# Performance work log

Hardware: AMD Instinct MI355X
Metric: run time of the kernel (lower is better)

The kernel has to match this reference:

```python
import jax, jax.numpy as jnp
import numpy as np

ALPHA = 0.2  # LeakyReLU negative slope
MASK_VAL = -1e12


def setup_inputs() -> dict:
    key = jax.random.key(0)
    k1, k2, k3, k4 = jax.random.split(key, 4)
    B, N, F_in, F_out = 16, 1024, 128, 64
    inp = jax.random.normal(k1, (B, N, F_in), dtype=jnp.float32)
    adj = jax.random.randint(k2, (B, N, N), 0, 2, dtype=jnp.int32)
    W = jax.random.normal(k3, (F_in, F_out), dtype=jnp.float32) * (1.414 / np.sqrt(F_in))
    a = jax.random.normal(k4, (2 * F_out, 1), dtype=jnp.float32) * (1.414 / np.sqrt(2 * F_out))
    return {"inp": inp, "adj": adj, "W": W, "a": a}


def reference(inp, adj, W, a):
    # inp: [B, N, F_in], adj: [B, N, N], W: [F_in, F_out], a: [2*F_out, 1]
    F_out = W.shape[1]
    h = jnp.einsum('bnf,fo->bno', inp, W)  # [B, N, F_out]
    # e_ij = LeakyReLU(a1 . h_i + a2 . h_j)  (equivalent to concat-then-matmul)
    a1 = a[:F_out, 0]  # [F_out]
    a2 = a[F_out:, 0]  # [F_out]
    e = jax.nn.leaky_relu(
        (h @ a1)[:, :, None] + (h @ a2)[:, None, :], negative_slope=ALPHA
    )  # [B, N, N]
    scores = jnp.where(adj > 0, e, MASK_VAL)
    attention = jax.nn.softmax(scores, axis=-1)  # [B, N, N]
    # dropout with p=0.0 / eval mode -> identity
    h_prime = jnp.einsum('bij,bjo->bio', attention, h)  # [B, N, F_out]
    return jax.nn.elu(h_prime)  # concat=True
```

## Files before the change

### kernel.cpp

```cpp
#include <hip/hip_runtime.h>
#include <cstdint>

#define BB   16
#define NN   1024
#define FIN  128
#define FOUT 64
#define ALPHA_S 0.2f
#define LOG2E 1.44269504f

typedef float    f32x4 __attribute__((ext_vector_type(4)));
typedef _Float16 half8 __attribute__((ext_vector_type(8)));
typedef _Float16 half4 __attribute__((ext_vector_type(4)));
typedef __fp16   pk2   __attribute__((ext_vector_type(2)));
typedef __fp16   pk4   __attribute__((ext_vector_type(4)));
typedef __fp16   pk8   __attribute__((ext_vector_type(8)));

__device__ __forceinline__ float fast_exp2(float x){
  float r; asm("v_exp_f32 %0, %1" : "=v"(r) : "v"(x)); return r;
}

__global__ __launch_bounds__(256) void k_proj(const float* __restrict__ inp,
                                              const float* __restrict__ W,
                                              const float* __restrict__ a,
                                              _Float16* __restrict__ hT,
                                              float* __restrict__ s1,
                                              float* __restrict__ s2){
  __shared__ float red1[4][16];
  __shared__ float red2[4][16];
  const int t = threadIdx.x;
  const int w = t >> 6, lane = t & 63;
  const int m16 = lane & 15, g = lane >> 4;
  const int i0 = blockIdx.x * 16;
  const int b  = i0 >> 10;
  const int j0 = i0 & 1023;
  const int c0 = w * 16;

  const float* arow = inp + (size_t)(i0 + m16) * FIN;

  f32x4 acc = {0.f, 0.f, 0.f, 0.f};
  #pragma unroll
  for (int kk = 0; kk < 4; ++kk){
    const int kbase = kk * 32 + g * 8;
    float4 av0 = *(const float4*)(arow + kbase);
    float4 av1 = *(const float4*)(arow + kbase + 4);
    const float av[8] = {av0.x, av0.y, av0.z, av0.w, av1.x, av1.y, av1.z, av1.w};
    half8 ah, al;
    #pragma unroll
    for (int j = 0; j < 8; ++j){
      _Float16 h = (_Float16)av[j];
      ah[j] = h;
      al[j] = (_Float16)(av[j] - (float)h);
    }
    half8 bh, bl;
    #pragma unroll
    for (int j = 0; j < 8; ++j){
      float wv = W[(kbase + j) * FOUT + c0 + m16];
      _Float16 h = (_Float16)wv;
      bh[j] = h;
      bl[j] = (_Float16)(wv - (float)h);
    }
    acc = __builtin_amdgcn_mfma_f32_16x16x32_f16(ah, bh, acc, 0, 0, 0);
    acc = __builtin_amdgcn_mfma_f32_16x16x32_f16(ah, bl, acc, 0, 0, 0);
    acc = __builtin_amdgcn_mfma_f32_16x16x32_f16(al, bh, acc, 0, 0, 0);
  }

  const float a1c = a[c0 + m16];
  const float a2c = a[FOUT + c0 + m16];
  f32x4 p1, p2;
  #pragma unroll
  for (int q = 0; q < 4; ++q){ p1[q] = acc[q] * a1c; p2[q] = acc[q] * a2c; }
  #pragma unroll
  for (int off = 1; off < 16; off <<= 1){
    #pragma unroll
    for (int q = 0; q < 4; ++q){
      p1[q] += __shfl_xor(p1[q], off, 64);
      p2[q] += __shfl_xor(p2[q], off, 64);
    }
  }
  if (m16 == 0){
    #pragma unroll
    for (int q = 0; q < 4; ++q){
      red1[w][g * 4 + q] = p1[q];
      red2[w][g * 4 + q] = p2[q];
    }
  }

  half4 hv;
  #pragma unroll
  for (int q = 0; q < 4; ++q) hv[q] = (_Float16)acc[q];
  size_t idx = (size_t)b * 65536 + (size_t)(j0 >> 5) * 2048
             + (size_t)(c0 + m16) * 32 + (size_t)(j0 & 31) + (size_t)g * 4;
  *(half4*)(hT + idx) = hv;

  __syncthreads();
  if (t < 16){
    s1[i0 + t] = (red1[0][t] + red1[1][t] + red1[2][t] + red1[3][t]) * LOG2E;
    s2[i0 + t] = (red2[0][t] + red2[1][t] + red2[2][t] + red2[3][t]) * LOG2E;
  }
}

__global__ __launch_bounds__(256, 4) void k_attn(const int* __restrict__ adj,
                                                 const _Float16* __restrict__ hT,
                                                 const float* __restrict__ s1,
                                                 const float* __restrict__ s2,
                                                 float* __restrict__ out){
  __shared__ float s2_s[NN];
  __shared__ float redmax[4][16];
  __shared__ float redl[4][16];
  __shared__ float csum[4][1088];

  const int t = threadIdx.x;
  const int w = t >> 6, lane = t & 63;
  const int m16 = lane & 15, g = lane >> 4;
  const int b  = blockIdx.x >> 6;
  const int i0 = (blockIdx.x & 63) * 16;
  const int jb = w * 256;

  *(float4*)&s2_s[jb + lane * 4] = *(const float4*)(s2 + b * NN + jb + lane * 4);

  const int* arow = adj + ((size_t)(b * NN + i0 + m16)) * NN + jb + g * 8;
  int4 A0[8], A1[8];
  #pragma unroll
  for (int kk = 0; kk < 8; ++kk){
    A0[kk] = *(const int4*)(arow + kk * 32);
    A1[kk] = *(const int4*)(arow + kk * 32 + 4);
  }

  const float s1i = s1[b * NN + i0 + m16];

  unsigned mask_lo = 0u, mask_hi = 0u;
  float mxp = -3.0e38f;
  #pragma unroll
  for (int kk = 0; kk < 8; ++kk){
    float4 sA = *(const float4*)&s2_s[jb + kk * 32 + g * 8];
    float4 sB = *(const float4*)&s2_s[jb + kk * 32 + g * 8 + 4];
    unsigned bits = 0u;
    bits |= (A0[kk].x > 0) ? 1u   : 0u;  mxp = fmaxf(mxp, A0[kk].x > 0 ? sA.x : -3.0e38f);
    bits |= (A0[kk].y > 0) ? 2u   : 0u;  mxp = fmaxf(mxp, A0[kk].y > 0 ? sA.y : -3.0e38f);
    bits |= (A0[kk].z > 0) ? 4u   : 0u;  mxp = fmaxf(mxp, A0[kk].z > 0 ? sA.z : -3.0e38f);
    bits |= (A0[kk].w > 0) ? 8u   : 0u;  mxp = fmaxf(mxp, A0[kk].w > 0 ? sA.w : -3.0e38f);
    bits |= (A1[kk].x > 0) ? 16u  : 0u;  mxp = fmaxf(mxp, A1[kk].x > 0 ? sB.x : -3.0e38f);
    bits |= (A1[kk].y > 0) ? 32u  : 0u;  mxp = fmaxf(mxp, A1[kk].y > 0 ? sB.y : -3.0e38f);
    bits |= (A1[kk].z > 0) ? 64u  : 0u;  mxp = fmaxf(mxp, A1[kk].z > 0 ? sB.z : -3.0e38f);
    bits |= (A1[kk].w > 0) ? 128u : 0u;  mxp = fmaxf(mxp, A1[kk].w > 0 ? sB.w : -3.0e38f);
    if (kk < 4) mask_lo |= bits << (kk * 8);
    else        mask_hi |= bits << ((kk - 4) * 8);
  }

  mxp = fmaxf(mxp, __shfl_xor(mxp, 16, 64));
  mxp = fmaxf(mxp, __shfl_xor(mxp, 32, 64));
  mxp = fmaxf(mxp, -1.0e30f);
  const float xm   = s1i + mxp;
  const float mrow = fmaxf(xm, ALPHA_S * xm);
  if (g == 0) redmax[w][m16] = mrow;
  const float s1m = s1i - mrow;
  const float c2  = ALPHA_S * s1i - mrow;

  f32x4 acc0 = {0,0,0,0}, acc1 = {0,0,0,0}, acc2 = {0,0,0,0}, acc3 = {0,0,0,0};
  float psum = 0.f;
  const _Float16* bhp = hT + (size_t)b * 65536 + (size_t)(w * 8) * 2048
                      + (size_t)m16 * 32 + (size_t)g * 8;

  #pragma unroll
  for (int kk = 0; kk < 8; ++kk){
    float4 sA = *(const float4*)&s2_s[jb + kk * 32 + g * 8];
    float4 sB = *(const float4*)&s2_s[jb + kk * 32 + g * 8 + 4];
    const unsigned bits = (kk < 4) ? (mask_lo >> (kk * 8)) : (mask_hi >> ((kk - 4) * 8));
    const float sv[8] = {sA.x, sA.y, sA.z, sA.w, sB.x, sB.y, sB.z, sB.w};
    float p[8];
    #pragma unroll
    for (int u = 0; u < 8; ++u){
      float e = fast_exp2(fmaxf(s1m + sv[u], fmaf(ALPHA_S, sv[u], c2)));
      p[u] = ((bits >> u) & 1u) ? e : 0.0f;
    }
    psum += ((p[0] + p[1]) + (p[2] + p[3])) + ((p[4] + p[5]) + (p[6] + p[7]));

    pk2 q0 = __builtin_amdgcn_cvt_pkrtz(p[0], p[1]);
    pk2 q1 = __builtin_amdgcn_cvt_pkrtz(p[2], p[3]);
    pk2 q2 = __builtin_amdgcn_cvt_pkrtz(p[4], p[5]);
    pk2 q3 = __builtin_amdgcn_cvt_pkrtz(p[6], p[7]);
    pk4 l0 = __builtin_shufflevector(q0, q1, 0, 1, 2, 3);
    pk4 l1 = __builtin_shufflevector(q2, q3, 0, 1, 2, 3);
    half8 af = __builtin_bit_cast(half8,
                 __builtin_shufflevector(l0, l1, 0, 1, 2, 3, 4, 5, 6, 7));

    half8 b0 = *(const half8*)(bhp + kk * 2048);
    half8 b1 = *(const half8*)(bhp + kk * 2048 + 512);
    half8 b2 = *(const half8*)(bhp + kk * 2048 + 1024);
    half8 b3 = *(const half8*)(bhp + kk * 2048 + 1536);
    acc0 = __builtin_amdgcn_mfma_f32_16x16x32_f16(af, b0, acc0, 0, 0, 0);
    acc1 = __builtin_amdgcn_mfma_f32_16x16x32_f16(af, b1, acc1, 0, 0, 0);
    acc2 = __builtin_amdgcn_mfma_f32_16x16x32_f16(af, b2, acc2, 0, 0, 0);
    acc3 = __builtin_amdgcn_mfma_f32_16x16x32_f16(af, b3, acc3, 0, 0, 0);
  }

  psum += __shfl_xor(psum, 16, 64);
  psum += __shfl_xor(psum, 32, 64);
  if (g == 0) redl[w][m16] = psum;

  #pragma unroll
  for (int q = 0; q < 4; ++q){
    csum[w][(g * 4 + q) * 68 +  0 + m16] = acc0[q];
    csum[w][(g * 4 + q) * 68 + 16 + m16] = acc1[q];
    csum[w][(g * 4 + q) * 68 + 32 + m16] = acc2[q];
    csum[w][(g * 4 + q) * 68 + 48 + m16] = acc3[q];
  }
  __syncthreads();

  const int r  = t >> 4;
  const int c4 = (t & 15) * 4;
  const float m0 = redmax[0][r], m1 = redmax[1][r];
  const float m2 = redmax[2][r], m3 = redmax[3][r];
  const float mg = fmaxf(fmaxf(m0, m1), fmaxf(m2, m3));
  const float f0 = fast_exp2(m0 - mg), f1 = fast_exp2(m1 - mg);
  const float f2 = fast_exp2(m2 - mg), f3 = fast_exp2(m3 - mg);

  f32x4 c0v = *(const f32x4*)&csum[0][r * 68 + c4];
  f32x4 c1v = *(const f32x4*)&csum[1][r * 68 + c4];
  f32x4 c2v = *(const f32x4*)&csum[2][r * 68 + c4];
  f32x4 c3v = *(const f32x4*)&csum[3][r * 68 + c4];
  f32x4 sum;
  #pragma unroll
  for (int u = 0; u < 4; ++u)
    sum[u] = c0v[u] * f0 + c1v[u] * f1 + c2v[u] * f2 + c3v[u] * f3;

  const float l = redl[0][r] * f0 + redl[1][r] * f1
                + redl[2][r] * f2 + redl[3][r] * f3;
  const float linv = (l > 0.f) ? __builtin_amdgcn_rcpf(l) : 0.f;
  f32x4 o;
  #pragma unroll
  for (int u = 0; u < 4; ++u){
    float v = sum[u] * linv;
    o[u] = v > 0.f ? v : __expf(v) - 1.0f;
  }
  *(f32x4*)(out + ((size_t)(b * NN + i0 + r)) * FOUT + c4) = o;
}

extern "C" void kernel_launch(void* const* d_in, const int* in_sizes, int n_in,
                              void* d_out, int out_size, void* d_ws, size_t ws_size,
                              hipStream_t stream) {
  (void)in_sizes; (void)n_in; (void)out_size; (void)ws_size;
  const float* inp = (const float*)d_in[0];
  const int*   adj = (const int*)d_in[1];
  const float* W   = (const float*)d_in[2];
  const float* a   = (const float*)d_in[3];
  float* outp = (float*)d_out;

  _Float16* hT = (_Float16*)d_ws;
  float* s1 = (float*)(hT + (size_t)BB * 65536);
  float* s2 = s1 + BB * NN;

  k_proj<<<BB * NN / 16, 256, 0, stream>>>(inp, W, a, hT, s1, s2);
  k_attn<<<BB * (NN / 16), 256, 0, stream>>>(adj, hT, s1, s2, outp);
}
```

Measured before the change: 115.1 us.

## Process four row tiles per projection block with W reuse and prefetch

The projection kernel now handles 64 rows per block instead of 16. It loads and splits W into fp16 hi/lo fragments once per block and reuses them across four 16-row tiles. The input rows for the next tile are prefetched into registers while the current tile computes. The reduction buffers are double-buffered so that one barrier per tile is enough, at the cost of higher register use and a grid four times smaller.

```diff
diff --git a/kernel.cpp b/kernel.cpp
--- a/kernel.cpp
+++ b/kernel.cpp
@@ -25,77 +25,105 @@
                                               _Float16* __restrict__ hT,
                                               float* __restrict__ s1,
                                               float* __restrict__ s2){
-  __shared__ float red1[4][16];
-  __shared__ float red2[4][16];
+  __shared__ float red1[2][4][16];
+  __shared__ float red2[2][4][16];
   const int t = threadIdx.x;
   const int w = t >> 6, lane = t & 63;
   const int m16 = lane & 15, g = lane >> 4;
-  const int i0 = blockIdx.x * 16;
-  const int b  = i0 >> 10;
-  const int j0 = i0 & 1023;
-  const int c0 = w * 16;
-
-  const float* arow = inp + (size_t)(i0 + m16) * FIN;
-
-  f32x4 acc = {0.f, 0.f, 0.f, 0.f};
+  const int bi0 = blockIdx.x * 64;
+  const int b   = bi0 >> 10;
+  const int c0  = w * 16;
+
+  half8 bhf[4], blf[4];
   #pragma unroll
   for (int kk = 0; kk < 4; ++kk){
     const int kbase = kk * 32 + g * 8;
-    float4 av0 = *(const float4*)(arow + kbase);
-    float4 av1 = *(const float4*)(arow + kbase + 4);
-    const float av[8] = {av0.x, av0.y, av0.z, av0.w, av1.x, av1.y, av1.z, av1.w};
-    half8 ah, al;
-    #pragma unroll
-    for (int j = 0; j < 8; ++j){
-      _Float16 h = (_Float16)av[j];
-      ah[j] = h;
-      al[j] = (_Float16)(av[j] - (float)h);
-    }
-    half8 bh, bl;
     #pragma unroll
     for (int j = 0; j < 8; ++j){
       float wv = W[(kbase + j) * FOUT + c0 + m16];
       _Float16 h = (_Float16)wv;
-      bh[j] = h;
-      bl[j] = (_Float16)(wv - (float)h);
-    }
-    acc = __builtin_amdgcn_mfma_f32_16x16x32_f16(ah, bh, acc, 0, 0, 0);
-    acc = __builtin_amdgcn_mfma_f32_16x16x32_f16(ah, bl, acc, 0, 0, 0);
-    acc = __builtin_amdgcn_mfma_f32_16x16x32_f16(al, bh, acc, 0, 0, 0);
+      bhf[kk][j] = h;
+      blf[kk][j] = (_Float16)(wv - (float)h);
+    }
   }
 
   const float a1c = a[c0 + m16];
   const float a2c = a[FOUT + c0 + m16];
-  f32x4 p1, p2;
-  #pragma unroll
-  for (int q = 0; q < 4; ++q){ p1[q] = acc[q] * a1c; p2[q] = acc[q] * a2c; }
-  #pragma unroll
-  for (int off = 1; off < 16; off <<= 1){
-    #pragma unroll
-    for (int q = 0; q < 4; ++q){
-      p1[q] += __shfl_xor(p1[q], off, 64);
-      p2[q] += __shfl_xor(p2[q], off, 64);
-    }
-  }
-  if (m16 == 0){
-    #pragma unroll
-    for (int q = 0; q < 4; ++q){
-      red1[w][g * 4 + q] = p1[q];
-      red2[w][g * 4 + q] = p2[q];
-    }
-  }
-
-  half4 hv;
-  #pragma unroll
-  for (int q = 0; q < 4; ++q) hv[q] = (_Float16)acc[q];
-  size_t idx = (size_t)b * 65536 + (size_t)(j0 >> 5) * 2048
-             + (size_t)(c0 + m16) * 32 + (size_t)(j0 & 31) + (size_t)g * 4;
-  *(half4*)(hT + idx) = hv;
-
-  __syncthreads();
-  if (t < 16){
-    s1[i0 + t] = (red1[0][t] + red1[1][t] + red1[2][t] + red1[3][t]) * LOG2E;
-    s2[i0 + t] = (red2[0][t] + red2[1][t] + red2[2][t] + red2[3][t]) * LOG2E;
+
+  float4 pv0[2][4], pv1[2][4];
+  {
+    const float* ar = inp + (size_t)(bi0 + m16) * FIN;
+    #pragma unroll
+    for (int kk = 0; kk < 4; ++kk){
+      pv0[0][kk] = *(const float4*)(ar + kk * 32 + g * 8);
+      pv1[0][kk] = *(const float4*)(ar + kk * 32 + g * 8 + 4);
+    }
+  }
+
+  #pragma unroll
+  for (int rt = 0; rt < 4; ++rt){
+    const int ph = rt & 1;
+    const int i0 = bi0 + rt * 16;
+    const int j0 = i0 & 1023;
+
+    if (rt < 3){
+      const float* ar = inp + (size_t)(i0 + 16 + m16) * FIN;
+      #pragma unroll
+      for (int kk = 0; kk < 4; ++kk){
+        pv0[ph ^ 1][kk] = *(const float4*)(ar + kk * 32 + g * 8);
+        pv1[ph ^ 1][kk] = *(const float4*)(ar + kk * 32 + g * 8 + 4);
+      }
+    }
+
+    f32x4 acc = {0.f, 0.f, 0.f, 0.f};
+    #pragma unroll
+    for (int kk = 0; kk < 4; ++kk){
+      const float4 a0 = pv0[ph][kk], a1 = pv1[ph][kk];
+      const float av[8] = {a0.x, a0.y, a0.z, a0.w, a1.x, a1.y, a1.z, a1.w};
+      half8 ah, al;
+      #pragma unroll
+      for (int j = 0; j < 8; ++j){
+        _Float16 h = (_Float16)av[j];
+        ah[j] = h;
+        al[j] = (_Float16)(av[j] - (float)h);
+      }
+      acc = __builtin_amdgcn_mfma_f32_16x16x32_f16(ah, bhf[kk], acc, 0, 0, 0);
+      acc = __builtin_amdgcn_mfma_f32_16x16x32_f16(ah, blf[kk], acc, 0, 0, 0);
+      acc = __builtin_amdgcn_mfma_f32_16x16x32_f16(al, bhf[kk], acc, 0, 0, 0);
+    }
+
+    half4 hv;
+    #pragma unroll
+    for (int q = 0; q < 4; ++q) hv[q] = (_Float16)acc[q];
+    size_t idx = (size_t)b * 65536 + (size_t)(j0 >> 5) * 2048
+               + (size_t)(c0 + m16) * 32 + (size_t)(j0 & 31) + (size_t)g * 4;
+    *(half4*)(hT + idx) = hv;
+
+    f32x4 p1, p2;
+    #pragma unroll
+    for (int q = 0; q < 4; ++q){ p1[q] = acc[q] * a1c; p2[q] = acc[q] * a2c; }
+    #pragma unroll
+    for (int off = 1; off < 16; off <<= 1){
+      #pragma unroll
+      for (int q = 0; q < 4; ++q){
+        p1[q] += __shfl_xor(p1[q], off, 64);
+        p2[q] += __shfl_xor(p2[q], off, 64);
+      }
+    }
+    if (m16 == 0){
+      #pragma unroll
+      for (int q = 0; q < 4; ++q){
+        red1[ph][w][g * 4 + q] = p1[q];
+        red2[ph][w][g * 4 + q] = p2[q];
+      }
+    }
+    __syncthreads();
+    if (t < 16){
+      s1[i0 + t] = (red1[ph][0][t] + red1[ph][1][t]
+                  + red1[ph][2][t] + red1[ph][3][t]) * LOG2E;
+      s2[i0 + t] = (red2[ph][0][t] + red2[ph][1][t]
+                  + red2[ph][2][t] + red2[ph][3][t]) * LOG2E;
+    }
   }
 }
 
@@ -250,6 +278,6 @@
   float* s1 = (float*)(hT + (size_t)BB * 65536);
   float* s2 = s1 + BB * NN;
 
-  k_proj<<<BB * NN / 16, 256, 0, stream>>>(inp, W, a, hT, s1, s2);
+  k_proj<<<BB * NN / 64, 256, 0, stream>>>(inp, W, a, hT, s1, s2);
   k_attn<<<BB * (NN / 16), 256, 0, stream>>>(adj, hT, s1, s2, outp);
 }
```

Result: no change. 115.9 us (+0.7%).

## Move adjacency bitmask packing from attention kernel into projection kernel

Applied to the files above, without the earlier changes.

The projection kernel now also reads the int32 adjacency matrix, packs each row into bitmasks, and writes them to workspace. The attention kernel reads the compact uint2 masks instead of the full adjacency. The intent is to move the large adjacency read into the projection kernel, where it can overlap with the projection loads and math, and to lighten the attention kernel. The total adjacency traffic stays the same, and a small extra mask write and read is added.

```diff
diff --git a/kernel.cpp b/kernel.cpp
--- a/kernel.cpp
+++ b/kernel.cpp
@@ -22,9 +22,11 @@
 __global__ __launch_bounds__(256) void k_proj(const float* __restrict__ inp,
                                               const float* __restrict__ W,
                                               const float* __restrict__ a,
+                                              const int* __restrict__ adj,
                                               _Float16* __restrict__ hT,
                                               float* __restrict__ s1,
-                                              float* __restrict__ s2){
+                                              float* __restrict__ s2,
+                                              uint2* __restrict__ msk){
   __shared__ float red1[4][16];
   __shared__ float red2[4][16];
   const int t = threadIdx.x;
@@ -35,29 +37,42 @@
   const int j0 = i0 & 1023;
   const int c0 = w * 16;
 
-  const float* arow = inp + (size_t)(i0 + m16) * FIN;
+  const float* arow_i = inp + (size_t)(i0 + m16) * FIN;
+  float4 iv0[4], iv1[4];
+  #pragma unroll
+  for (int kk = 0; kk < 4; ++kk){
+    iv0[kk] = *(const float4*)(arow_i + kk * 32 + g * 8);
+    iv1[kk] = *(const float4*)(arow_i + kk * 32 + g * 8 + 4);
+  }
+  float wv[4][8];
+  #pragma unroll
+  for (int kk = 0; kk < 4; ++kk){
+    #pragma unroll
+    for (int j = 0; j < 8; ++j)
+      wv[kk][j] = W[(kk * 32 + g * 8 + j) * FOUT + c0 + m16];
+  }
+  const int* arow_a = adj + (size_t)(i0 + m16) * NN + w * 256 + g * 8;
+  int4 A0[8], A1[8];
+  #pragma unroll
+  for (int kk = 0; kk < 8; ++kk){
+    A0[kk] = *(const int4*)(arow_a + kk * 32);
+    A1[kk] = *(const int4*)(arow_a + kk * 32 + 4);
+  }
 
   f32x4 acc = {0.f, 0.f, 0.f, 0.f};
   #pragma unroll
   for (int kk = 0; kk < 4; ++kk){
-    const int kbase = kk * 32 + g * 8;
-    float4 av0 = *(const float4*)(arow + kbase);
-    float4 av1 = *(const float4*)(arow + kbase + 4);
-    const float av[8] = {av0.x, av0.y, av0.z, av0.w, av1.x, av1.y, av1.z, av1.w};
-    half8 ah, al;
+    const float av[8] = {iv0[kk].x, iv0[kk].y, iv0[kk].z, iv0[kk].w,
+                         iv1[kk].x, iv1[kk].y, iv1[kk].z, iv1[kk].w};
+    half8 ah, al, bh, bl;
     #pragma unroll
     for (int j = 0; j < 8; ++j){
       _Float16 h = (_Float16)av[j];
       ah[j] = h;
       al[j] = (_Float16)(av[j] - (float)h);
-    }
-    half8 bh, bl;
-    #pragma unroll
-    for (int j = 0; j < 8; ++j){
-      float wv = W[(kbase + j) * FOUT + c0 + m16];
-      _Float16 h = (_Float16)wv;
-      bh[j] = h;
-      bl[j] = (_Float16)(wv - (float)h);
+      _Float16 hw = (_Float16)wv[kk][j];
+      bh[j] = hw;
+      bl[j] = (_Float16)(wv[kk][j] - (float)hw);
     }
     acc = __builtin_amdgcn_mfma_f32_16x16x32_f16(ah, bh, acc, 0, 0, 0);
     acc = __builtin_amdgcn_mfma_f32_16x16x32_f16(ah, bl, acc, 0, 0, 0);
@@ -97,9 +112,26 @@
     s1[i0 + t] = (red1[0][t] + red1[1][t] + red1[2][t] + red1[3][t]) * LOG2E;
     s2[i0 + t] = (red2[0][t] + red2[1][t] + red2[2][t] + red2[3][t]) * LOG2E;
   }
-}
-
-__global__ __launch_bounds__(256, 4) void k_attn(const int* __restrict__ adj,
+
+  unsigned mask_lo = 0u, mask_hi = 0u;
+  #pragma unroll
+  for (int kk = 0; kk < 8; ++kk){
+    unsigned bits = 0u;
+    bits |= (A0[kk].x > 0) ? 1u   : 0u;
+    bits |= (A0[kk].y > 0) ? 2u   : 0u;
+    bits |= (A0[kk].z > 0) ? 4u   : 0u;
+    bits |= (A0[kk].w > 0) ? 8u   : 0u;
+    bits |= (A1[kk].x > 0) ? 16u  : 0u;
+    bits |= (A1[kk].y > 0) ? 32u  : 0u;
+    bits |= (A1[kk].z > 0) ? 64u  : 0u;
+    bits |= (A1[kk].w > 0) ? 128u : 0u;
+    if (kk < 4) mask_lo |= bits << (kk * 8);
+    else        mask_hi |= bits << ((kk - 4) * 8);
+  }
+  msk[(size_t)blockIdx.x * 256 + t] = make_uint2(mask_lo, mask_hi);
+}
+
+__global__ __launch_bounds__(256, 4) void k_attn(const uint2* __restrict__ msk,
                                                  const _Float16* __restrict__ hT,
                                                  const float* __restrict__ s1,
                                                  const float* __restrict__ s2,
@@ -118,33 +150,23 @@
 
   *(float4*)&s2_s[jb + lane * 4] = *(const float4*)(s2 + b * NN + jb + lane * 4);
 
-  const int* arow = adj + ((size_t)(b * NN + i0 + m16)) * NN + jb + g * 8;
-  int4 A0[8], A1[8];
-  #pragma unroll
-  for (int kk = 0; kk < 8; ++kk){
-    A0[kk] = *(const int4*)(arow + kk * 32);
-    A1[kk] = *(const int4*)(arow + kk * 32 + 4);
-  }
-
+  const uint2 mk  = msk[(size_t)blockIdx.x * 256 + t];
   const float s1i = s1[b * NN + i0 + m16];
 
-  unsigned mask_lo = 0u, mask_hi = 0u;
   float mxp = -3.0e38f;
   #pragma unroll
   for (int kk = 0; kk < 8; ++kk){
     float4 sA = *(const float4*)&s2_s[jb + kk * 32 + g * 8];
     float4 sB = *(const float4*)&s2_s[jb + kk * 32 + g * 8 + 4];
-    unsigned bits = 0u;
-    bits |= (A0[kk].x > 0) ? 1u   : 0u;  mxp = fmaxf(mxp, A0[kk].x > 0 ? sA.x : -3.0e38f);
-    bits |= (A0[kk].y > 0) ? 2u   : 0u;  mxp = fmaxf(mxp, A0[kk].y > 0 ? sA.y : -3.0e38f);
-    bits |= (A0[kk].z > 0) ? 4u   : 0u;  mxp = fmaxf(mxp, A0[kk].z > 0 ? sA.z : -3.0e38f);
-    bits |= (A0[kk].w > 0) ? 8u   : 0u;  mxp = fmaxf(mxp, A0[kk].w > 0 ? sA.w : -3.0e38f);
-    bits |= (A1[kk].x > 0) ? 16u  : 0u;  mxp = fmaxf(mxp, A1[kk].x > 0 ? sB.x : -3.0e38f);
-    bits |= (A1[kk].y > 0) ? 32u  : 0u;  mxp = fmaxf(mxp, A1[kk].y > 0 ? sB.y : -3.0e38f);
-    bits |= (A1[kk].z > 0) ? 64u  : 0u;  mxp = fmaxf(mxp, A1[kk].z > 0 ? sB.z : -3.0e38f);
-    bits |= (A1[kk].w > 0) ? 128u : 0u;  mxp = fmaxf(mxp, A1[kk].w > 0 ? sB.w : -3.0e38f);
-    if (kk < 4) mask_lo |= bits << (kk * 8);
-    else        mask_hi |= bits << ((kk - 4) * 8);
+    const unsigned bits = (kk < 4) ? (mk.x >> (kk * 8)) : (mk.y >> ((kk - 4) * 8));
+    mxp = fmaxf(mxp, (bits & 1u)   ? sA.x : -3.0e38f);
+    mxp = fmaxf(mxp, (bits & 2u)   ? sA.y : -3.0e38f);
+    mxp = fmaxf(mxp, (bits & 4u)   ? sA.z : -3.0e38f);
+    mxp = fmaxf(mxp, (bits & 8u)   ? sA.w : -3.0e38f);
+    mxp = fmaxf(mxp, (bits & 16u)  ? sB.x : -3.0e38f);
+    mxp = fmaxf(mxp, (bits & 32u)  ? sB.y : -3.0e38f);
+    mxp = fmaxf(mxp, (bits & 64u)  ? sB.z : -3.0e38f);
+    mxp = fmaxf(mxp, (bits & 128u) ? sB.w : -3.0e38f);
   }
 
   mxp = fmaxf(mxp, __shfl_xor(mxp, 16, 64));
@@ -165,7 +187,7 @@
   for (int kk = 0; kk < 8; ++kk){
     float4 sA = *(const float4*)&s2_s[jb + kk * 32 + g * 8];
     float4 sB = *(const float4*)&s2_s[jb + kk * 32 + g * 8 + 4];
-    const unsigned bits = (kk < 4) ? (mask_lo >> (kk * 8)) : (mask_hi >> ((kk - 4) * 8));
+    const unsigned bits = (kk < 4) ? (mk.x >> (kk * 8)) : (mk.y >> ((kk - 4) * 8));
     const float sv[8] = {sA.x, sA.y, sA.z, sA.w, sB.x, sB.y, sB.z, sB.w};
     float p[8];
     #pragma unroll
@@ -249,7 +271,8 @@
   _Float16* hT = (_Float16*)d_ws;
   float* s1 = (float*)(hT + (size_t)BB * 65536);
   float* s2 = s1 + BB * NN;
-
-  k_proj<<<BB * NN / 16, 256, 0, stream>>>(inp, W, a, hT, s1, s2);
-  k_attn<<<BB * (NN / 16), 256, 0, stream>>>(adj, hT, s1, s2, outp);
-}
+  uint2* msk = (uint2*)(s2 + BB * NN);
+
+  k_proj<<<BB * NN / 16, 256, 0, stream>>>(inp, W, a, adj, hT, s1, s2, msk);
+  k_attn<<<BB * (NN / 16), 256, 0, stream>>>(msk, hT, s1, s2, outp);
+}
```

Measured after the change: 118.4 us. 2.9% more time.
